# Optimization experiments

Hardware: AMD Instinct MI355X
Metric: run time of the kernel (lower is better)

## Reference

```python
import jax, jax.numpy as jnp
import numpy as np

N = 50000   # nodes
E = 800000  # edges (avg degree 16)
D = 128     # in_features == out_features


def setup_inputs() -> dict:
    key = jax.random.key(0)
    k1, k2, k3, k4, k5 = jax.random.split(key, 5)
    inputs = jax.random.normal(k1, (N, D), jnp.float32)
    h0 = jax.random.normal(k2, (N, D), jnp.float32)
    edge_src = jax.random.randint(k3, (E,), 0, N, jnp.int32)
    edge_dst = jax.random.randint(k4, (E,), 0, N, jnp.int32)
    stdv = 1.0 / np.sqrt(D)  # reset_parameters: uniform(-stdv, stdv), stdv = 1/sqrt(out_features)
    weight = jax.random.uniform(k5, (D, D), jnp.float32, -stdv, stdv)
    return {"inputs": inputs, "edge_src": edge_src, "edge_dst": edge_dst,
            "h0": h0, "weight": weight, "lamda": 0.5, "alpha": 0.1, "l": 4}


def reference(inputs, edge_src, edge_dst, h0, weight, lamda, alpha, l):
    n = inputs.shape[0]
    theta = np.float32(np.log(lamda / l + 1.0))
    # in-degrees (edges point src -> dst), clamped to >= 1
    deg = jax.ops.segment_sum(jnp.ones(edge_src.shape[0], inputs.dtype), edge_dst, num_segments=n)
    dinv = jnp.maximum(deg, 1.0) ** -0.5  # [N]
    # symmetric-normalized SpMM: h_agg = D^-1/2 A D^-1/2 h
    msg = inputs[edge_src] * dinv[edge_src][:, None]           # [E, D] gather + scale
    h_acc = jax.ops.segment_sum(msg, edge_dst, num_segments=n)  # [N, D] scatter-sum
    hi = h_acc * dinv[:, None]
    # variant=False: convex combine with initial residual h0
    support = (1.0 - alpha) * hi + alpha * h0
    out = theta * (support @ weight) + (1.0 - theta) * support
    # residual=True
    return out + inputs
```

## Files before the change

### kernel.cpp

```cpp
#include <hip/hip_runtime.h>
#include <math.h>

#define D 128
#define P_MAX 32
#define OCAP 65536
#define CHUNK 2048
#define NSLICE 4
#define SXP 140

using bf16x8 = __attribute__((ext_vector_type(8))) short;
using f32x4  = __attribute__((ext_vector_type(4))) float;

__device__ __forceinline__ float int_or_float(const void* p) {
    int iv = *(const int*)p;
    if (iv > -1000000 && iv < 1000000) return (float)iv;
    return __int_as_float(iv);
}

__device__ __forceinline__ unsigned bf16_rne(float f) {
    unsigned u = __float_as_uint(f);
    return (u + 0x7fffu + ((u >> 16) & 1u)) >> 16;
}
__device__ __forceinline__ unsigned pack_bf2(float a, float b) {
    return bf16_rne(a) | (bf16_rne(b) << 16);
}


__global__ __launch_bounds__(256) void k_prep(
        const int* __restrict__ src, const int* __restrict__ dst,
        int* __restrict__ deg, int* __restrict__ planes,
        int* __restrict__ cnt, int2* __restrict__ opairs,
        const float4* __restrict__ x4,
        uint2* __restrict__ xs8, float* __restrict__ s0,
        float* __restrict__ sxs,
        const float* __restrict__ W, uint4* __restrict__ wmt,
        const float* __restrict__ lamda_p, const void* __restrict__ l_p,
        int E, int n, int NBR, int NBQ) {
    const int t = threadIdx.x;
    int bid = blockIdx.x;

    if (bid < NBR) {
        const int slice = bid & (NSLICE - 1);
        const int chunk = bid / NSLICE;
        int base = chunk * CHUNK;
        int end = base + CHUNK;
        if (end > E) end = E;
        for (int i = base + t; i < end; i += 256) {
            int tt = dst[i];
            if (((tt >> 4) & (NSLICE - 1)) == slice) {
                int s = src[i];
                int rk = atomicAdd(&deg[tt], 1);
                if (rk < P_MAX) {
                    planes[(size_t)tt * P_MAX + rk] = s;
                } else {
                    int o = atomicAdd(cnt, 1);
                    if (o < OCAP) opairs[o] = make_int2(s, tt);
                }
            }
        }
        return;
    }
    bid -= NBR;

    if (bid < NBQ) {
        int gid = bid * 256 + t;
        int r = gid >> 4;
        if (r >= n) return;
        int q = gid & 15;
        float4 v0 = x4[(size_t)r * 32 + q * 2];
        float4 v1 = x4[(size_t)r * 32 + q * 2 + 1];
        float f[8] = {v0.x, v0.y, v0.z, v0.w, v1.x, v1.y, v1.z, v1.w};
        float m = 0.f;
        #pragma unroll
        for (int i = 0; i < 8; ++i) m = fmaxf(m, fabsf(f[i]));
        #pragma unroll
        for (int off = 1; off < 16; off <<= 1)
            m = fmaxf(m, __shfl_xor(m, off, 16));
        float s = m * (1.f / 127.f);
        float rs = m > 0.f ? 127.f / m : 0.f;
        unsigned b[8];
        #pragma unroll
        for (int i = 0; i < 8; ++i)
            b[i] = (unsigned)(__float2int_rn(f[i] * rs) + 128);
        uint2 o;
        o.x = b[0] | (b[1] << 8) | (b[2] << 16) | (b[3] << 24);
        o.y = b[4] | (b[5] << 8) | (b[6] << 16) | (b[7] << 24);
        xs8[(size_t)r * 16 + q] = o;
        if (q == 0) s0[r] = s;
        return;
    }
    bid -= NBQ;
    if (bid == 0) {
        if (t < 32) ((unsigned*)xs8)[(int)t - 32] = 0u;
        if (t == 32) sxs[-1] = 0.f;
    }
    int tid = bid * 256 + t;
    float lamda = *lamda_p;
    float lf = int_or_float(l_p);
    float theta = logf(lamda / lf + 1.0f);
    float omt = 1.0f - theta;
    int ct = tid >> 8, kb = (tid >> 6) & 3, kg = (tid >> 4) & 3, lc = tid & 15;
    int c = ct * 16 + lc;
    int k0 = kb * 32 + kg * 8;
    float v[8];
    #pragma unroll
    for (int j = 0; j < 8; ++j) {
        float wv = theta * W[(size_t)(k0 + j) * D + c];
        if (k0 + j == c) wv += omt;
        v[j] = wv;
    }
    uint4 o;
    o.x = pack_bf2(v[0], v[1]);
    o.y = pack_bf2(v[2], v[3]);
    o.z = pack_bf2(v[4], v[5]);
    o.w = pack_bf2(v[6], v[7]);
    wmt[tid] = o;
}

__global__ __launch_bounds__(256) void k_post(const int* __restrict__ deg,
                                              const float* __restrict__ s0,
                                              float* __restrict__ sxs,
                                              int* __restrict__ planes, int n) {
    int gid = blockIdx.x * 256 + threadIdx.x;
    int r = gid >> 3;
    if (r >= n) return;
    int j = gid & 7;
    int d = deg[r];
    int dcl = d < P_MAX ? d : P_MAX;
    int c8 = (dcl + 7) & ~7;
    if (dcl + j < c8) planes[(size_t)r * P_MAX + dcl + j] = -1;
    if (j == 0) {
        int dd = d < 1 ? 1 : d;
        sxs[r] = s0[r] * rsqrtf((float)dd);
    }
}

__device__ __forceinline__ void accq(float* a, uint2 v, float s) {
    a[0] += (float)(v.x & 0xffu) * s;
    a[1] += (float)((v.x >> 8) & 0xffu) * s;
    a[2] += (float)((v.x >> 16) & 0xffu) * s;
    a[3] += (float)(v.x >> 24) * s;
    a[4] += (float)(v.y & 0xffu) * s;
    a[5] += (float)((v.y >> 8) & 0xffu) * s;
    a[6] += (float)((v.y >> 16) & 0xffu) * s;
    a[7] += (float)(v.y >> 24) * s;
}

__global__ __launch_bounds__(256) void k_fused(
        const uint2* __restrict__ xs8, const float* __restrict__ sxs,
        const float* __restrict__ s0, const int* __restrict__ planes,
        const int* __restrict__ deg, const int* __restrict__ cnt,
        const int2* __restrict__ opairs, const float* __restrict__ h0,
        const float* __restrict__ alpha_p, const uint4* __restrict__ wmt,
        float* __restrict__ out, int n) {
    __shared__ uint4 sS[256];
    __shared__ float sX[16 * SXP];
    const int t = threadIdx.x;
    const int base = blockIdx.x * 16;

    {
        const int g = t >> 4;
        const int q = t & 15;
        int r = base + g;
        int rc = r < n ? r : 0;
        int d = r < n ? deg[rc] : 0;
        int dc = d < P_MAX ? d : P_MAX;
        const char* xsb = (const char*)xs8;
        const float4* h04 = (const float4*)h0;
        float4 hb0 = h04[(size_t)rc * 32 + q * 2];
        float4 hb1 = h04[(size_t)rc * 32 + q * 2 + 1];
        uint2 own = *(const uint2*)(xsb + (size_t)rc * 128 + q * 8);
        float s0r = s0[rc];
        const int4* prow = (const int4*)(planes + (size_t)rc * P_MAX);
        float a0[8] = {}, a1[8] = {}, a2[8] = {}, a3[8] = {};
        float ssum = 0.f;
        for (int p = 0; p < dc; p += 8) {
            int4 w0 = prow[(p >> 2) + 0];
            int4 w1 = prow[(p >> 2) + 1];
            float c0 = sxs[w0.x], c1 = sxs[w0.y], c2 = sxs[w0.z], c3 = sxs[w0.w];
            float c4 = sxs[w1.x], c5 = sxs[w1.y], c6 = sxs[w1.z], c7 = sxs[w1.w];
            uint2 v0 = *(const uint2*)(xsb + (long)w0.x * 128 + q * 8);
            uint2 v1 = *(const uint2*)(xsb + (long)w0.y * 128 + q * 8);
            uint2 v2 = *(const uint2*)(xsb + (long)w0.z * 128 + q * 8);
            uint2 v3 = *(const uint2*)(xsb + (long)w0.w * 128 + q * 8);
            uint2 v4 = *(const uint2*)(xsb + (long)w1.x * 128 + q * 8);
            uint2 v5 = *(const uint2*)(xsb + (long)w1.y * 128 + q * 8);
            uint2 v6 = *(const uint2*)(xsb + (long)w1.z * 128 + q * 8);
            uint2 v7 = *(const uint2*)(xsb + (long)w1.w * 128 + q * 8);
            accq(a0, v0, c0);
            accq(a1, v1, c1);
            accq(a2, v2, c2);
            accq(a3, v3, c3);
            accq(a0, v4, c4);
            accq(a1, v5, c5);
            accq(a2, v6, c6);
            accq(a3, v7, c7);
            ssum += ((c0 + c1) + (c2 + c3)) + ((c4 + c5) + (c6 + c7));
        }
        if (d > P_MAX) {
            int c = *cnt;
            if (c > OCAP) c = OCAP;
            for (int i = 0; i < c; ++i) {
                int2 pr = opairs[i];
                if (pr.y == r) {
                    float cs = sxs[pr.x];
                    uint2 v = *(const uint2*)(xsb + (long)pr.x * 128 + q * 8);
                    accq(a0, v, cs);
                    ssum += cs;
                }
            }
        }
        {
            float xi[8];
            xi[0] = ((float)(own.x & 0xffu) - 128.f) * s0r;
            xi[1] = ((float)((own.x >> 8) & 0xffu) - 128.f) * s0r;
            xi[2] = ((float)((own.x >> 16) & 0xffu) - 128.f) * s0r;
            xi[3] = ((float)(own.x >> 24) - 128.f) * s0r;
            xi[4] = ((float)(own.y & 0xffu) - 128.f) * s0r;
            xi[5] = ((float)((own.y >> 8) & 0xffu) - 128.f) * s0r;
            xi[6] = ((float)((own.y >> 16) & 0xffu) - 128.f) * s0r;
            xi[7] = ((float)(own.y >> 24) - 128.f) * s0r;
            *(float4*)&sX[g * SXP + q * 8] =
                make_float4(xi[0], xi[1], xi[2], xi[3]);
            *(float4*)&sX[g * SXP + q * 8 + 4] =
                make_float4(xi[4], xi[5], xi[6], xi[7]);
        }
        float di = rsqrtf((float)(d < 1 ? 1 : d));
        float alpha = *alpha_p;
        float ca = (1.0f - alpha) * di;
        float corr = 128.f * ssum;
        float t0 = ca * (((a0[0] + a1[0]) + (a2[0] + a3[0])) - corr) + alpha * hb0.x;
        float t1 = ca * (((a0[1] + a1[1]) + (a2[1] + a3[1])) - corr) + alpha * hb0.y;
        float t2 = ca * (((a0[2] + a1[2]) + (a2[2] + a3[2])) - corr) + alpha * hb0.z;
        float t3 = ca * (((a0[3] + a1[3]) + (a2[3] + a3[3])) - corr) + alpha * hb0.w;
        float t4 = ca * (((a0[4] + a1[4]) + (a2[4] + a3[4])) - corr) + alpha * hb1.x;
        float t5 = ca * (((a0[5] + a1[5]) + (a2[5] + a3[5])) - corr) + alpha * hb1.y;
        float t6 = ca * (((a0[6] + a1[6]) + (a2[6] + a3[6])) - corr) + alpha * hb1.z;
        float t7 = ca * (((a0[7] + a1[7]) + (a2[7] + a3[7])) - corr) + alpha * hb1.w;
        uint4 o;
        o.x = pack_bf2(t0, t1);
        o.y = pack_bf2(t2, t3);
        o.z = pack_bf2(t4, t5);
        o.w = pack_bf2(t6, t7);
        sS[g * 16 + (q ^ (g & 7))] = o;
    }
    __syncthreads();

    const int lane = t & 63;
    const int wv = t >> 6;
    const int lr = lane & 15;
    const int kg = lane >> 4;

    bf16x8 a[4];
    #pragma unroll
    for (int kb = 0; kb < 4; ++kb)
        a[kb] = ((const bf16x8*)sS)[lr * 16 + ((kb * 4 + kg) ^ (lr & 7))];

    const bf16x8* wfr = (const bf16x8*)wmt;
    #pragma unroll
    for (int j = 0; j < 2; ++j) {
        int ct = wv * 2 + j;
        f32x4 acc = (f32x4){0.f, 0.f, 0.f, 0.f};
        #pragma unroll
        for (int kb = 0; kb < 4; ++kb) {
            bf16x8 b = wfr[ct * 256 + kb * 64 + lane];
            acc = __builtin_amdgcn_mfma_f32_16x16x32_bf16(a[kb], b, acc, 0, 0, 0);
        }
        int c = ct * 16 + lr;
        #pragma unroll
        for (int reg = 0; reg < 4; ++reg) {
            int tr = kg * 4 + reg;
            int rr = base + tr;
            if (rr < n) {
                size_t off = (size_t)rr * D + c;
                out[off] = acc[reg] + sX[tr * SXP + c];
            }
        }
    }
}


__global__ __launch_bounds__(256) void k_deg(const int* __restrict__ dst,
                                             int* __restrict__ deg, int E) {
    int i = blockIdx.x * 256 + threadIdx.x;
    if (i < E) atomicAdd(&deg[dst[i]], 1);
}

__global__ __launch_bounds__(256) void k_dinv(int* dd, int n) {
    int i = blockIdx.x * 256 + threadIdx.x;
    if (i < n) {
        int d = dd[i];
        if (d < 1) d = 1;
        ((float*)dd)[i] = rsqrtf((float)d);
    }
}

__global__ __launch_bounds__(256) void k_scan1(const int* __restrict__ deg,
                                               int* __restrict__ bsum, int n) {
    __shared__ int red[256];
    int b = blockIdx.x, t = threadIdx.x;
    int base = b * 1024;
    int s = 0;
    #pragma unroll
    for (int i = 0; i < 4; ++i) {
        int idx = base + i * 256 + t;
        if (idx < n) s += deg[idx];
    }
    red[t] = s;
    __syncthreads();
    for (int k = 128; k > 0; k >>= 1) {
        if (t < k) red[t] += red[t + k];
        __syncthreads();
    }
    if (t == 0) bsum[b] = red[0];
}

__global__ void k_scan2(const int* __restrict__ bsum, int* __restrict__ boff,
                        int* __restrict__ offsets, int nb, int n) {
    if (threadIdx.x == 0) {
        int acc = 0;
        for (int i = 0; i < nb; ++i) { boff[i] = acc; acc += bsum[i]; }
        offsets[n] = acc;
    }
}

__global__ __launch_bounds__(256) void k_scan3(int* __restrict__ deg,
                                               const int* __restrict__ boff,
                                               int* __restrict__ offsets,
                                               int* __restrict__ cursor, int n) {
    __shared__ int ls[256];
    int b = blockIdx.x, t = threadIdx.x;
    int base = b * 1024 + t * 4;
    int v[4];
    #pragma unroll
    for (int i = 0; i < 4; ++i) v[i] = (base + i < n) ? deg[base + i] : 0;
    int mysum = v[0] + v[1] + v[2] + v[3];
    ls[t] = mysum;
    __syncthreads();
    for (int k = 1; k < 256; k <<= 1) {
        int add = (t >= k) ? ls[t - k] : 0;
        __syncthreads();
        ls[t] += add;
        __syncthreads();
    }
    int p = boff[b] + ls[t] - mysum;
    #pragma unroll
    for (int i = 0; i < 4; ++i) {
        if (base + i < n) {
            offsets[base + i] = p;
            cursor[base + i] = p;
            int d = v[i] < 1 ? 1 : v[i];
            ((float*)deg)[base + i] = rsqrtf((float)d);
        }
        p += v[i];
    }
}

__global__ __launch_bounds__(256) void k_csr(const int* __restrict__ src,
                                             const int* __restrict__ dst,
                                             int* __restrict__ cursor,
                                             int* __restrict__ csr_src, int E) {
    int i = blockIdx.x * 256 + threadIdx.x;
    if (i < E) {
        int pos = atomicAdd(&cursor[dst[i]], 1);
        csr_src[pos] = src[i];
    }
}

__global__ __launch_bounds__(256) void k_gather(const float4* __restrict__ x4,
                                                const int* __restrict__ csr_src,
                                                const int* __restrict__ offsets,
                                                const float* __restrict__ dinv,
                                                float4* __restrict__ hacc, int n) {
    int idx = blockIdx.x * 256 + threadIdx.x;
    int r = idx >> 5;
    if (r >= n) return;
    int q = idx & 31;
    int e0 = offsets[r], e1 = offsets[r + 1];
    float4 a0 = make_float4(0.f, 0.f, 0.f, 0.f);
    float4 a1 = make_float4(0.f, 0.f, 0.f, 0.f);
    float4 a2 = make_float4(0.f, 0.f, 0.f, 0.f);
    float4 a3 = make_float4(0.f, 0.f, 0.f, 0.f);
    int e = e0;
    for (; e + 4 <= e1; e += 4) {
        int s0 = csr_src[e + 0];
        int s1 = csr_src[e + 1];
        int s2 = csr_src[e + 2];
        int s3 = csr_src[e + 3];
        float c0 = dinv[s0], c1 = dinv[s1], c2 = dinv[s2], c3 = dinv[s3];
        float4 v0 = x4[(size_t)s0 * (D / 4) + q];
        float4 v1 = x4[(size_t)s1 * (D / 4) + q];
        float4 v2 = x4[(size_t)s2 * (D / 4) + q];
        float4 v3 = x4[(size_t)s3 * (D / 4) + q];
        a0.x += v0.x * c0; a0.y += v0.y * c0; a0.z += v0.z * c0; a0.w += v0.w * c0;
        a1.x += v1.x * c1; a1.y += v1.y * c1; a1.z += v1.z * c1; a1.w += v1.w * c1;
        a2.x += v2.x * c2; a2.y += v2.y * c2; a2.z += v2.z * c2; a2.w += v2.w * c2;
        a3.x += v3.x * c3; a3.y += v3.y * c3; a3.z += v3.z * c3; a3.w += v3.w * c3;
    }
    for (; e < e1; ++e) {
        int s = csr_src[e];
        float c = dinv[s];
        float4 v = x4[(size_t)s * (D / 4) + q];
        a0.x += v.x * c; a0.y += v.y * c; a0.z += v.z * c; a0.w += v.w * c;
    }
    float4 acc;
    acc.x = (a0.x + a1.x) + (a2.x + a3.x);
    acc.y = (a0.y + a1.y) + (a2.y + a3.y);
    acc.z = (a0.z + a1.z) + (a2.z + a3.z);
    acc.w = (a0.w + a1.w) + (a2.w + a3.w);
    hacc[(size_t)r * (D / 4) + q] = acc;
}

__global__ __launch_bounds__(256) void k_scatter(const float4* __restrict__ x4,
                                                 const int* __restrict__ src,
                                                 const int* __restrict__ dst,
                                                 const float* __restrict__ dinv,
                                                 float* hacc, int E) {
    int idx = blockIdx.x * 256 + threadIdx.x;
    int e = idx >> 5;
    if (e >= E) return;
    int q = idx & 31;
    int s = src[e];
    int t = dst[e];
    float sc = dinv[s];
    float4 v = x4[(size_t)s * (D / 4) + q];
    float* h = hacc + (size_t)t * D + q * 4;
    unsafeAtomicAdd(h + 0, v.x * sc);
    unsafeAtomicAdd(h + 1, v.y * sc);
    unsafeAtomicAdd(h + 2, v.z * sc);
    unsafeAtomicAdd(h + 3, v.w * sc);
}

__global__ __launch_bounds__(256) void k_final(float* io,
                                               const float* __restrict__ dinv,
                                               const float* __restrict__ h0,
                                               const float* __restrict__ x,
                                               const float* __restrict__ W,
                                               const float* __restrict__ lamda_p,
                                               const float* __restrict__ alpha_p,
                                               const void* __restrict__ l_p,
                                               int n) {
    __shared__ float sW[D * D];
    __shared__ float sSup[32][D];
    const int t = threadIdx.x;

    {
        const float4* W4 = (const float4*)W;
        float4* sW4 = (float4*)sW;
        #pragma unroll
        for (int i = 0; i < (D * D / 4) / 256; ++i)
            sW4[i * 256 + t] = W4[i * 256 + t];
    }

    const float alpha = *alpha_p;
    const float lamda = *lamda_p;
    const float lf = int_or_float(l_p);
    const float theta = logf(lamda / lf + 1.0f);
    const float omt = 1.0f - theta;
    const float oma = 1.0f - alpha;

    const int base = blockIdx.x * 32;

    {
        const float4* hacc4 = (const float4*)io;
        const float4* h04 = (const float4*)h0;
        #pragma unroll
        for (int i = 0; i < 4; ++i) {
            int v = i * 256 + t;
            int tr = v >> 5;
            int q = v & 31;
            int r = base + tr;
            float4 sup = make_float4(0.f, 0.f, 0.f, 0.f);
            if (r < n) {
                float ca = oma * dinv[r];
                float4 a = hacc4[(size_t)r * (D / 4) + q];
                float4 b = h04[(size_t)r * (D / 4) + q];
                sup.x = ca * a.x + alpha * b.x;
                sup.y = ca * a.y + alpha * b.y;
                sup.z = ca * a.z + alpha * b.z;
                sup.w = ca * a.w + alpha * b.w;
            }
            *(float4*)&sSup[tr][q * 4] = sup;
        }
    }
    __syncthreads();

    const int cg = t & 31;
    const int rb = t >> 5;
    float acc[4][4] = {};
    const float4* sW4 = (const float4*)sW;
    #pragma unroll 4
    for (int k = 0; k < D; ++k) {
        float4 w = sW4[k * 32 + cg];
        #pragma unroll
        for (int j = 0; j < 4; ++j) {
            float s = sSup[rb * 4 + j][k];
            acc[j][0] += s * w.x;
            acc[j][1] += s * w.y;
            acc[j][2] += s * w.z;
            acc[j][3] += s * w.w;
        }
    }

    #pragma unroll
    for (int j = 0; j < 4; ++j) {
        int tr = rb * 4 + j;
        int r = base + tr;
        if (r < n) {
            float4 xi = ((const float4*)x)[(size_t)r * (D / 4) + cg];
            float4 sp = *(const float4*)&sSup[tr][cg * 4];
            float4 o;
            o.x = theta * acc[j][0] + omt * sp.x + xi.x;
            o.y = theta * acc[j][1] + omt * sp.y + xi.y;
            o.z = theta * acc[j][2] + omt * sp.z + xi.z;
            o.w = theta * acc[j][3] + omt * sp.w + xi.w;
            ((float4*)io)[(size_t)r * (D / 4) + cg] = o;
        }
    }
}


extern "C" void kernel_launch(void* const* d_in, const int* in_sizes, int n_in,
                              void* d_out, int out_size, void* d_ws, size_t ws_size,
                              hipStream_t stream) {
    const float* x = (const float*)d_in[0];
    const int* esrc = (const int*)d_in[1];
    const int* edst = (const int*)d_in[2];
    const float* h0 = (const float*)d_in[3];
    const float* W = (const float*)d_in[4];
    const float* lamda_p = (const float*)d_in[5];
    const float* alpha_p = (const float*)d_in[6];
    const void* l_p = d_in[7];

    const int E = in_sizes[1];
    const int n = in_sizes[0] / D;

    char* w = (char*)d_ws;

    size_t o_deg = 0;
    size_t o_cnt = ((size_t)n * 4 + 15) & ~15ull;
    size_t o_op  = o_cnt + 16;
    size_t o_x8g = (o_op + (size_t)OCAP * 8 + 15) & ~15ull;
    size_t o_sxg = (o_x8g + 128 + (size_t)n * 128 + 15) & ~15ull;
    size_t o_s0  = (o_sxg + 16 + (size_t)n * 4 + 15) & ~15ull;
    size_t o_wmt = (o_s0 + (size_t)n * 4 + 15) & ~15ull;
    size_t o_pl  = (o_wmt + 32768 + 15) & ~15ull;
    size_t need1 = o_pl + (size_t)P_MAX * n * 4;

    if (ws_size >= need1) {
        int* deg = (int*)(w + o_deg);
        int* cnt = (int*)(w + o_cnt);
        int2* opairs = (int2*)(w + o_op);
        uint2* xs8 = (uint2*)(w + o_x8g + 128);
        float* sxs = (float*)(w + o_sxg + 16);
        float* s0 = (float*)(w + o_s0);
        uint4* wmt = (uint4*)(w + o_wmt);
        int* planes = (int*)(w + o_pl);

        hipMemsetAsync(w, 0, o_cnt + 16, stream);

        int chunks = (E + CHUNK - 1) / CHUNK;
        int NBR = chunks * NSLICE;
        int NBQ = ((size_t)n * 16 + 255) / 256;
        k_prep<<<NBR + NBQ + 8, 256, 0, stream>>>(
            esrc, edst, deg, planes, cnt, opairs,
            (const float4*)x, xs8, s0, sxs, W, wmt, lamda_p, l_p,
            E, n, NBR, NBQ);
        k_post<<<((size_t)n * 8 + 255) / 256, 256, 0, stream>>>(
            deg, s0, sxs, planes, n);
        k_fused<<<(n + 15) / 16, 256, 0, stream>>>(
            xs8, sxs, s0, planes, deg, cnt, opairs, h0, alpha_p, wmt,
            (float*)d_out, n);
        return;
    }

    const int nb = (n + 1023) / 1024;
    size_t t_deg = 0;
    size_t t_off = (t_deg + (size_t)n * 4 + 15) & ~15ull;
    size_t t_cur = (t_off + (size_t)(n + 1) * 4 + 15) & ~15ull;
    size_t t_bs  = (t_cur + (size_t)n * 4 + 15) & ~15ull;
    size_t t_bo  = (t_bs + (size_t)nb * 4 + 15) & ~15ull;
    size_t t_csr = (t_bo + (size_t)nb * 4 + 15) & ~15ull;
    size_t need2 = t_csr + (size_t)E * 4;

    int* deg = (int*)(w + t_deg);
    float* dinv = (float*)(w + t_deg);

    hipMemsetAsync(deg, 0, (size_t)n * sizeof(int), stream);
    k_deg<<<(E + 255) / 256, 256, 0, stream>>>(edst, deg, E);

    if (ws_size >= need2 && nb <= 1024) {
        int* offsets = (int*)(w + t_off);
        int* cursor  = (int*)(w + t_cur);
        int* bsum    = (int*)(w + t_bs);
        int* boff    = (int*)(w + t_bo);
        int* csr_src = (int*)(w + t_csr);

        k_scan1<<<nb, 256, 0, stream>>>(deg, bsum, n);
        k_scan2<<<1, 64, 0, stream>>>(bsum, boff, offsets, nb, n);
        k_scan3<<<nb, 256, 0, stream>>>(deg, boff, offsets, cursor, n);
        k_csr<<<(E + 255) / 256, 256, 0, stream>>>(esrc, edst, cursor, csr_src, E);
        k_gather<<<((size_t)n * 32 + 255) / 256, 256, 0, stream>>>(
            (const float4*)x, csr_src, offsets, dinv, (float4*)d_out, n);
    } else {
        k_dinv<<<(n + 255) / 256, 256, 0, stream>>>(deg, n);
        hipMemsetAsync(d_out, 0, (size_t)n * D * sizeof(float), stream);
        k_scatter<<<((size_t)E * 32 + 255) / 256, 256, 0, stream>>>(
            (const float4*)x, esrc, edst, dinv, (float*)d_out, E);
    }

    k_final<<<(n + 31) / 32, 256, 0, stream>>>(
        (float*)d_out, dinv, h0, x, W, lamda_p, alpha_p, l_p, n);
}
```

Before: 89.45 us.

## Replace global-atomic edge binning with two-pass bucketed sort into LDS planes

Edge binning becomes two passes. In the first, each block histograms its chunk of edges by destination bucket of 256 rows in shared memory, scans the counts, and writes the staged pairs contiguously into per-bucket global regions. In the second, one block per bucket builds the padded neighbor planes and degrees in LDS and writes them out coalesced, which also absorbs the old post kernel. This removes scattered per-edge global atomics on deg and scattered plane writes, at the cost of an extra pairs buffer, an overflow list, and a limit of 256 buckets.

```diff
diff --git a/kernel.cpp b/kernel.cpp
--- a/kernel.cpp
+++ b/kernel.cpp
@@ -4,8 +4,9 @@
 #define D 128
 #define P_MAX 32
 #define OCAP 65536
+#define CAPA 16384
 #define CHUNK 2048
-#define NSLICE 4
+#define BCAP 4608
 #define SXP 140
 
 using bf16x8 = __attribute__((ext_vector_type(8))) short;
@@ -26,36 +27,66 @@
 }
 
 
-__global__ __launch_bounds__(256) void k_prep(
+__global__ __launch_bounds__(256) void k_prepA(
         const int* __restrict__ src, const int* __restrict__ dst,
-        int* __restrict__ deg, int* __restrict__ planes,
-        int* __restrict__ cnt, int2* __restrict__ opairs,
+        int* __restrict__ bcur, int2* __restrict__ pairs,
+        int* __restrict__ cntA, int2* __restrict__ listA,
         const float4* __restrict__ x4,
         uint2* __restrict__ xs8, float* __restrict__ s0,
         float* __restrict__ sxs,
         const float* __restrict__ W, uint4* __restrict__ wmt,
         const float* __restrict__ lamda_p, const void* __restrict__ l_p,
-        int E, int n, int NBR, int NBQ) {
+        int E, int n, int NBUK, int NBR, int NBQ) {
     const int t = threadIdx.x;
     int bid = blockIdx.x;
 
     if (bid < NBR) {
-        const int slice = bid & (NSLICE - 1);
-        const int chunk = bid / NSLICE;
-        int base = chunk * CHUNK;
-        int end = base + CHUNK;
-        if (end > E) end = E;
-        for (int i = base + t; i < end; i += 256) {
-            int tt = dst[i];
-            if (((tt >> 4) & (NSLICE - 1)) == slice) {
-                int s = src[i];
-                int rk = atomicAdd(&deg[tt], 1);
-                if (rk < P_MAX) {
-                    planes[(size_t)tt * P_MAX + rk] = s;
-                } else {
-                    int o = atomicAdd(cnt, 1);
-                    if (o < OCAP) opairs[o] = make_int2(s, tt);
-                }
+        __shared__ int2 stag[CHUNK];
+        __shared__ int hist[256], scn[256], lb[256], gb[256];
+        hist[t] = 0;
+        __syncthreads();
+        int base = bid * CHUNK;
+        int2 e[8];
+        int bk[8], rk[8];
+        #pragma unroll
+        for (int i = 0; i < 8; ++i) {
+            int idx = base + i * 256 + t;
+            if (idx < E) {
+                e[i].x = src[idx];
+                e[i].y = dst[idx];
+                bk[i] = e[i].y >> 8;
+                rk[i] = atomicAdd(&hist[bk[i]], 1);
+            } else {
+                bk[i] = -1;
+            }
+        }
+        __syncthreads();
+        scn[t] = hist[t];
+        __syncthreads();
+        for (int k = 1; k < 256; k <<= 1) {
+            int add = (t >= k) ? scn[t - k] : 0;
+            __syncthreads();
+            scn[t] += add;
+            __syncthreads();
+        }
+        lb[t] = scn[t] - hist[t];
+        if (t < NBUK && hist[t] > 0) gb[t] = atomicAdd(&bcur[t], hist[t]);
+        else gb[t] = 0;
+        __syncthreads();
+        #pragma unroll
+        for (int i = 0; i < 8; ++i)
+            if (bk[i] >= 0) stag[lb[bk[i]] + rk[i]] = e[i];
+        __syncthreads();
+        int total = scn[255];
+        for (int p = t; p < total; p += 256) {
+            int2 pr = stag[p];
+            int b = pr.y >> 8;
+            int slot = gb[b] + (p - lb[b]);
+            if (slot < BCAP) {
+                pairs[(size_t)b * BCAP + slot] = pr;
+            } else {
+                int o = atomicAdd(cntA, 1);
+                if (o < CAPA) listA[o] = pr;
             }
         }
         return;
@@ -117,21 +148,65 @@
     wmt[tid] = o;
 }
 
-__global__ __launch_bounds__(256) void k_post(const int* __restrict__ deg,
-                                              const float* __restrict__ s0,
-                                              float* __restrict__ sxs,
-                                              int* __restrict__ planes, int n) {
-    int gid = blockIdx.x * 256 + threadIdx.x;
-    int r = gid >> 3;
-    if (r >= n) return;
-    int j = gid & 7;
-    int d = deg[r];
-    int dcl = d < P_MAX ? d : P_MAX;
-    int c8 = (dcl + 7) & ~7;
-    if (dcl + j < c8) planes[(size_t)r * P_MAX + dcl + j] = -1;
-    if (j == 0) {
-        int dd = d < 1 ? 1 : d;
-        sxs[r] = s0[r] * rsqrtf((float)dd);
+__global__ __launch_bounds__(256) void k_prepB(
+        const int2* __restrict__ pairs, const int* __restrict__ bcur,
+        const int* __restrict__ cntA, const int2* __restrict__ listA,
+        int* __restrict__ deg, int* __restrict__ planes,
+        float* __restrict__ sxs, const float* __restrict__ s0,
+        int* __restrict__ cntB, int2* __restrict__ listB, int n) {
+    __shared__ int pl[256 * P_MAX];
+    __shared__ int dg[256];
+    const int t = threadIdx.x;
+    const int b = blockIdx.x;
+    #pragma unroll
+    for (int i = t; i < 256 * P_MAX; i += 256) pl[i] = -1;
+    dg[t] = 0;
+    __syncthreads();
+
+    int count = bcur[b];
+    if (count > BCAP) count = BCAP;
+    const int2* bp = pairs + (size_t)b * BCAP;
+    for (int i = t; i < count; i += 256) {
+        int2 pr = bp[i];
+        int lr = pr.y & 255;
+        int rk = atomicAdd(&dg[lr], 1);
+        if (rk < P_MAX) {
+            pl[lr * P_MAX + rk] = pr.x;
+        } else {
+            int o = atomicAdd(cntB, 1);
+            if (o < OCAP) listB[o] = pr;
+        }
+    }
+    int ca = *cntA;
+    if (ca > CAPA) ca = CAPA;
+    for (int i = t; i < ca; i += 256) {
+        int2 pr = listA[i];
+        if ((pr.y >> 8) == b) {
+            int lr = pr.y & 255;
+            int rk = atomicAdd(&dg[lr], 1);
+            if (rk < P_MAX) {
+                pl[lr * P_MAX + rk] = pr.x;
+            } else {
+                int o = atomicAdd(cntB, 1);
+                if (o < OCAP) listB[o] = pr;
+            }
+        }
+    }
+    __syncthreads();
+
+    int r0 = b * 256;
+    for (int i = t; i < 256 * P_MAX; i += 256) {
+        int r = r0 + (i >> 5);
+        if (r < n) planes[(size_t)r * P_MAX + (i & 31)] = pl[i];
+    }
+    {
+        int r = r0 + t;
+        if (r < n) {
+            int d = dg[t];
+            deg[r] = d;
+            int dd = d < 1 ? 1 : d;
+            sxs[r] = s0[r] * rsqrtf((float)dd);
+        }
     }
 }
 
@@ -534,42 +609,50 @@
 
     const int E = in_sizes[1];
     const int n = in_sizes[0] / D;
+    const int NBUK = (n + 255) >> 8;
 
     char* w = (char*)d_ws;
 
-    size_t o_deg = 0;
-    size_t o_cnt = ((size_t)n * 4 + 15) & ~15ull;
-    size_t o_op  = o_cnt + 16;
-    size_t o_x8g = (o_op + (size_t)OCAP * 8 + 15) & ~15ull;
+    size_t o_bc  = 0;
+    size_t o_ca  = ((size_t)NBUK * 4 + 15) & ~15ull;
+    size_t o_cb  = o_ca + 16;
+    size_t o_la  = o_cb + 16;
+    size_t o_lb  = (o_la + (size_t)CAPA * 8 + 15) & ~15ull;
+    size_t o_deg = (o_lb + (size_t)OCAP * 8 + 15) & ~15ull;
+    size_t o_x8g = (o_deg + (size_t)n * 4 + 15) & ~15ull;
     size_t o_sxg = (o_x8g + 128 + (size_t)n * 128 + 15) & ~15ull;
     size_t o_s0  = (o_sxg + 16 + (size_t)n * 4 + 15) & ~15ull;
     size_t o_wmt = (o_s0 + (size_t)n * 4 + 15) & ~15ull;
     size_t o_pl  = (o_wmt + 32768 + 15) & ~15ull;
-    size_t need1 = o_pl + (size_t)P_MAX * n * 4;
-
-    if (ws_size >= need1) {
+    size_t o_pr  = (o_pl + (size_t)n * P_MAX * 4 + 15) & ~15ull;
+    size_t need1 = o_pr + (size_t)NBUK * BCAP * 8;
+
+    if (ws_size >= need1 && NBUK <= 256) {
+        int* bcur = (int*)(w + o_bc);
+        int* cntA = (int*)(w + o_ca);
+        int* cntB = (int*)(w + o_cb);
+        int2* listA = (int2*)(w + o_la);
+        int2* listB = (int2*)(w + o_lb);
         int* deg = (int*)(w + o_deg);
-        int* cnt = (int*)(w + o_cnt);
-        int2* opairs = (int2*)(w + o_op);
         uint2* xs8 = (uint2*)(w + o_x8g + 128);
         float* sxs = (float*)(w + o_sxg + 16);
         float* s0 = (float*)(w + o_s0);
         uint4* wmt = (uint4*)(w + o_wmt);
         int* planes = (int*)(w + o_pl);
-
-        hipMemsetAsync(w, 0, o_cnt + 16, stream);
-
-        int chunks = (E + CHUNK - 1) / CHUNK;
-        int NBR = chunks * NSLICE;
+        int2* pairs = (int2*)(w + o_pr);
+
+        hipMemsetAsync(w, 0, o_la, stream);
+
+        int NBR = (E + CHUNK - 1) / CHUNK;
         int NBQ = ((size_t)n * 16 + 255) / 256;
-        k_prep<<<NBR + NBQ + 8, 256, 0, stream>>>(
-            esrc, edst, deg, planes, cnt, opairs,
+        k_prepA<<<NBR + NBQ + 8, 256, 0, stream>>>(
+            esrc, edst, bcur, pairs, cntA, listA,
             (const float4*)x, xs8, s0, sxs, W, wmt, lamda_p, l_p,
-            E, n, NBR, NBQ);
-        k_post<<<((size_t)n * 8 + 255) / 256, 256, 0, stream>>>(
-            deg, s0, sxs, planes, n);
+            E, n, NBUK, NBR, NBQ);
+        k_prepB<<<NBUK, 256, 0, stream>>>(
+            pairs, bcur, cntA, listA, deg, planes, sxs, s0, cntB, listB, n);
         k_fused<<<(n + 15) / 16, 256, 0, stream>>>(
-            xs8, sxs, s0, planes, deg, cnt, opairs, h0, alpha_p, wmt,
+            xs8, sxs, s0, planes, deg, cntB, listB, h0, alpha_p, wmt,
             (float*)d_out, n);
         return;
     }
```

Result: faster. 75.36 us (-15.8%).
